# Performance work log

Measured on AMD Instinct MI355X. Metric: run time of the kernel, lower is better.

Reference implementation:

```python
import jax, jax.numpy as jnp
import numpy as np

WEIGHT_FACTOR = 0.8


def _pairwise_l2(f):
    # ||a-b|| via GEMM trick: ||a||^2 + ||b||^2 - 2 a.b, avoiding the [N,N,D] blowup.
    sqn = jnp.sum(f * f, axis=1)                      # [N]
    sq = sqn[:, None] + sqn[None, :] - 2.0 * (f @ f.T)  # [N,N]
    sq = jnp.maximum(sq, 0.0)
    pos = sq > 0
    # safe sqrt: subgradient 0 at zero distance (matches torch.norm at 0)
    return jnp.where(pos, jnp.sqrt(jnp.where(pos, sq, 1.0)), 0.0)


def _mse(a, b):
    d = a - b
    return jnp.mean(d * d)


def setup_inputs() -> dict:
    key = jax.random.key(0)
    ks = jax.random.split(key, 8)
    N, D, C = 4096, 256, 1000
    return {
        "pred": jax.random.normal(ks[0], (N, C), dtype=jnp.float32),
        "target": jax.random.normal(ks[1], (N, C), dtype=jnp.float32),
        "pred_f0": jax.random.normal(ks[2], (N, D), dtype=jnp.float32),
        "pred_f1": jax.random.normal(ks[3], (N, D), dtype=jnp.float32),
        "pred_f2": jax.random.normal(ks[4], (N, D), dtype=jnp.float32),
        "target_f0": jax.random.normal(ks[5], (N, D), dtype=jnp.float32),
        "target_f1": jax.random.normal(ks[6], (N, D), dtype=jnp.float32),
        "target_f2": jax.random.normal(ks[7], (N, D), dtype=jnp.float32),
    }


def reference(pred, target, pred_f0, pred_f1, pred_f2, target_f0, target_f1, target_f2):
    pred_feats = (pred_f0, pred_f1, pred_f2)
    target_feats = (target_f0, target_f1, target_f2)
    num_features = len(pred_feats)

    label_loss = _mse(pred, target)
    feature_loss = 0.0
    for pf, tf in zip(pred_feats, target_feats):
        feature_loss = feature_loss + _mse(_pairwise_l2(pf), _pairwise_l2(tf))
    return (1.0 - WEIGHT_FACTOR) * label_loss + WEIGHT_FACTOR * feature_loss / num_features
```

## Files before the change

kernel.cpp:

```cpp
#include <hip/hip_runtime.h>
#include <stdint.h>

#define NR 4096
#define DD 256
#define NC_TOT 4096000
#define TILES 32
#define NTRI 528
#define NBLK_GRAM 512

typedef float f32x4 __attribute__((ext_vector_type(4)));
typedef unsigned char u8;

#define WS_MSEP_OFF  256
#define WS_FEATP_OFF 16384
#define WS_SQN_OFF   32768
#define WS_FP8_OFF   131072

#define GBAR()     asm volatile("s_barrier" ::: "memory")
#define WAIT_VM(N) asm volatile("s_waitcnt vmcnt(" #N ")" ::: "memory")

__global__ __launch_bounds__(256) void prep_mse_kernel(
    const float* __restrict__ m0, const float* __restrict__ m1,
    const float* __restrict__ m2, const float* __restrict__ m3,
    const float* __restrict__ m4, const float* __restrict__ m5,
    const float4* __restrict__ pred, const float4* __restrict__ target,
    u8* __restrict__ q8, float* __restrict__ sqn, float* __restrict__ msep,
    unsigned* __restrict__ cnt)
{
    __shared__ float sr[4];
    const int t = threadIdx.x, w = t >> 6, lane = t & 63;
    const int y = blockIdx.y;
    if (y == 0 && blockIdx.x == 0 && t == 0) *cnt = 0u;

    if (y < 6) {
        const float* mp = m0;
        if (y == 1) mp = m1;
        else if (y == 2) mp = m2;
        else if (y == 3) mp = m3;
        else if (y == 4) mp = m4;
        else if (y == 5) mp = m5;
        const int R = blockIdx.x * 4 + w;
        const int P = R >> 7, rr = R & 127;
        const float4* src = (const float4*)(mp + (size_t)R * DD);
        float4 v = src[lane];
        float ss = v.x * v.x + v.y * v.y + v.z * v.z + v.w * v.w;
        unsigned lo = __builtin_amdgcn_cvt_pk_fp8_f32(v.x, v.y, 0u, false);
        unsigned hi = __builtin_amdgcn_cvt_pk_fp8_f32(v.z, v.w, 0u, false);
        unsigned packed = (lo & 0xffffu) | (hi << 16);
        size_t idx = ((size_t)(y * 32 + P) << 15)
                     + (size_t)(lane >> 1) * 1024 + rr * 8 + (lane & 1) * 4;
        *(unsigned*)(q8 + idx) = packed;
        #pragma unroll
        for (int off = 32; off; off >>= 1) ss += __shfl_down(ss, off);
        if (lane == 0) sqn[(size_t)y * NR + R] = ss;
    } else {
        const int b2 = (y - 6) * 1024 + blockIdx.x;
        float s = 0.f;
        for (int i = b2 * 256 + t; i < NC_TOT / 4; i += 2048 * 256) {
            float4 x = pred[i], yv = target[i];
            float dx = x.x - yv.x, dy = x.y - yv.y;
            float dz = x.z - yv.z, dw = x.w - yv.w;
            s += dx * dx + dy * dy + dz * dz + dw * dw;
        }
        #pragma unroll
        for (int off = 32; off; off >>= 1) s += __shfl_down(s, off);
        if (lane == 0) sr[w] = s;
        __syncthreads();
        if (t == 0) msep[b2] = sr[0] + sr[1] + sr[2] + sr[3];
    }
}

#define COMPUTE_STAGE(BI, ACC)                                                 \
  do {                                                                         \
    const u8* tA_ = &buf[BI][0];                                               \
    const u8* tB_ = &buf[BI][16384];                                           \
    __builtin_amdgcn_s_setprio(1);                                             \
    _Pragma("unroll")                                                          \
    for (int kc = 0; kc < 4; kc++) {                                           \
      const int gg = kc * 4 + quad;                                            \
      long a_[4], b_[2];                                                       \
      _Pragma("unroll")                                                        \
      for (int mi = 0; mi < 4; mi++)                                           \
        a_[mi] = *(const long*)&tA_[gg * 1024 + (wm * 64 + mi * 16 + l16) * 8];\
      _Pragma("unroll")                                                        \
      for (int ni = 0; ni < 2; ni++)                                           \
        b_[ni] = *(const long*)&tB_[gg * 1024 + (wn * 32 + ni * 16 + l16) * 8];\
      _Pragma("unroll")                                                        \
      for (int mi = 0; mi < 4; mi++)                                           \
        _Pragma("unroll")                                                      \
        for (int ni = 0; ni < 2; ni++)                                         \
          ACC[mi][ni] = __builtin_amdgcn_mfma_f32_16x16x32_fp8_fp8(            \
              a_[mi], b_[ni], ACC[mi][ni], 0, 0, 0);                           \
    }                                                                          \
    __builtin_amdgcn_s_setprio(0);                                             \
  } while (0)

#define RESET_ACC()                                                            \
  do {                                                                         \
    _Pragma("unroll")                                                          \
    for (int a4 = 0; a4 < 4; a4++)                                             \
      _Pragma("unroll")                                                        \
      for (int b2 = 0; b2 < 2; b2++) {                                         \
        accp[a4][b2] = f32x4{0.f, 0.f, 0.f, 0.f};                              \
        acct[a4][b2] = f32x4{0.f, 0.f, 0.f, 0.f};                              \
      }                                                                        \
  } while (0)

__global__ __launch_bounds__(512, 4) void gram_loss_kernel(
    const u8* __restrict__ q8, const float* __restrict__ sqn,
    float* __restrict__ featp, const float* __restrict__ msep,
    unsigned* __restrict__ cnt, float* __restrict__ out)
{
    __shared__ u8 buf[2][32768];
    __shared__ float s_red[8];
    __shared__ int s_last;

    const int xcd = blockIdx.x & 7, slot = blockIdx.x >> 3;
    const int t = threadIdx.x;
    const int w = t >> 6, lane = t & 63;
    const int wm = w >> 2, wn = w & 3;
    const int quad = lane >> 4, l16 = lane & 15;
    const char* qb = (const char*)q8;

    auto tile_of = [&](int k, int& f, int& ti, int& tj) -> bool {
        int rs = (slot + k * 21 + xcd * 9) & 63;
        int idx = rs + (k << 6), lin;
        if (xcd < 6) {
            if (idx >= 196) return false;
            f = xcd >> 1; lin = (xcd & 1) + 2 * idx;
        } else {
            if (idx >= 204) return false;
            int rr = (xcd - 6) + 2 * idx;
            f = rr / 136; lin = 392 + rr - f * 136;
        }
        int a = 0, rem = lin;
        while (rem >= TILES - a) { rem -= TILES - a; a++; }
        ti = a; tj = a + rem;
        return true;
    };

    auto prefetch = [&](int b, int f, int ti, int tj, int tgt, int kk) {
        const int m = f + 3 * tgt;
        const size_t bA = ((size_t)(m * 32 + ti)) << 15;
        const size_t bB = ((size_t)(m * 32 + tj)) << 15;
        const char* g = qb + ((w < 4) ? bA : bB) + kk * 16384
                        + (w & 3) * 4096 + lane * 16;
        char* l = (char*)&buf[b][0] + ((w < 4) ? 0 : 16384) + (w & 3) * 4096;
        #pragma unroll
        for (int i = 0; i < 4; i++)
            __builtin_amdgcn_global_load_lds(
                (const __attribute__((address_space(1))) void*)(g + i * 1024),
                (__attribute__((address_space(3))) void*)(l + i * 1024), 16, 0, 0);
    };

    f32x4 accp[4][2], acct[4][2];
    RESET_ACC();

    float local = 0.f;

    int fc, tic, tjc;
    tile_of(0, fc, tic, tjc);
    prefetch(0, fc, tic, tjc, 0, 0);
    prefetch(1, fc, tic, tjc, 0, 1);

    int k = 0;
    while (true) {
        WAIT_VM(4); GBAR();
        COMPUTE_STAGE(0, accp);
        GBAR();

        prefetch(0, fc, tic, tjc, 1, 0);
        WAIT_VM(4); GBAR();
        COMPUTE_STAGE(1, accp);
        GBAR();

        prefetch(1, fc, tic, tjc, 1, 1);
        WAIT_VM(4); GBAR();
        COMPUTE_STAGE(0, acct);
        GBAR();

        int fn, tin, tjn;
        const bool more = tile_of(k + 1, fn, tin, tjn);
        if (more) { prefetch(0, fn, tin, tjn, 0, 0); WAIT_VM(4); }
        else      { WAIT_VM(0); }
        GBAR();
        COMPUTE_STAGE(1, acct);
        GBAR();
        if (more) prefetch(1, fn, tin, tjn, 0, 1);

        {
            const float* sqp = sqn + (size_t)fc * NR;
            const float* sqt = sqn + (size_t)(3 + fc) * NR;
            const bool diag = (tic == tjc);
            float tl = 0.f;
            #pragma unroll
            for (int mi = 0; mi < 4; mi++) {
                const int i0 = wm * 64 + mi * 16 + quad * 4;
                const f32x4 sip = *(const f32x4*)(sqp + tic * 128 + i0);
                const f32x4 sit = *(const f32x4*)(sqt + tic * 128 + i0);
                #pragma unroll
                for (int ni = 0; ni < 2; ni++) {
                    const int j_loc = wn * 32 + ni * 16 + l16;
                    const float spj = sqp[tjc * 128 + j_loc];
                    const float stj = sqt[tjc * 128 + j_loc];
                    const f32x4 gp = accp[mi][ni], gt = acct[mi][ni];
                    #pragma unroll
                    for (int r = 0; r < 4; r++) {
                        float dp2 = fmaxf(fmaf(-2.f, gp[r], sip[r] + spj), 0.f);
                        float dt2 = fmaxf(fmaf(-2.f, gt[r], sit[r] + stj), 0.f);
                        if (diag && (i0 + r == j_loc)) { dp2 = 0.f; dt2 = 0.f; }
                        float sq = __builtin_amdgcn_sqrtf(dp2 * dt2);
                        tl += fmaf(-2.f, sq, dp2 + dt2);
                    }
                }
            }
            local += diag ? tl : 2.f * tl;
            RESET_ACC();
        }
        if (!more) break;
        k++;
        fc = fn; tic = tin; tjc = tjn;
    }

    #pragma unroll
    for (int off = 32; off; off >>= 1) local += __shfl_down(local, off);
    if (lane == 0) s_red[w] = local;
    __syncthreads();
    if (t == 0) {
        float bs = 0.f;
        #pragma unroll
        for (int i = 0; i < 8; i++) bs += s_red[i];
        featp[blockIdx.x] = bs;
        __threadfence();
        unsigned old = atomicAdd(cnt, 1u);
        s_last = (old == NBLK_GRAM - 1) ? 1 : 0;
    }
    __syncthreads();

    if (s_last) {
        __threadfence();
        float s2 = 0.f, m2 = 0.f;
        for (int i = t; i < NBLK_GRAM; i += 512) s2 += featp[i];
        for (int i = t; i < 2048; i += 512) m2 += msep[i];
        #pragma unroll
        for (int off = 32; off; off >>= 1) {
            s2 += __shfl_down(s2, off);
            m2 += __shfl_down(m2, off);
        }
        __shared__ float fr[8], mr[8];
        if (lane == 0) { fr[w] = s2; mr[w] = m2; }
        __syncthreads();
        if (t == 0) {
            float fs = 0.f, ms = 0.f;
            #pragma unroll
            for (int i = 0; i < 8; i++) { fs += fr[i]; ms += mr[i]; }
            out[0] = 0.2f * (ms / (float)NC_TOT) +
                     (0.8f / 3.0f) * (fs / ((float)NR * (float)NR));
        }
    }
}

extern "C" void kernel_launch(void* const* d_in, const int* in_sizes, int n_in,
                              void* d_out, int out_size, void* d_ws, size_t ws_size,
                              hipStream_t stream) {
    unsigned* cnt  = (unsigned*)d_ws;
    float* msep    = (float*)((char*)d_ws + WS_MSEP_OFF);
    float* featp   = (float*)((char*)d_ws + WS_FEATP_OFF);
    float* sqn     = (float*)((char*)d_ws + WS_SQN_OFF);
    u8* q8         = (u8*)((char*)d_ws + WS_FP8_OFF);

    prep_mse_kernel<<<dim3(1024, 8), 256, 0, stream>>>(
        (const float*)d_in[2], (const float*)d_in[3], (const float*)d_in[4],
        (const float*)d_in[5], (const float*)d_in[6], (const float*)d_in[7],
        (const float4*)d_in[0], (const float4*)d_in[1], q8, sqn, msep, cnt);

    gram_loss_kernel<<<NBLK_GRAM, 512, 0, stream>>>(
        q8, sqn, featp, msep, cnt, (float*)d_out);
}
```

Baseline: 142.4 us.

## Split gram tiles into 128x64 halves with 256-thread blocks and 768 blocks

```diff
diff --git a/kernel.cpp b/kernel.cpp
--- a/kernel.cpp
+++ b/kernel.cpp
@@ -6,7 +6,7 @@
 #define NC_TOT 4096000
 #define TILES 32
 #define NTRI 528
-#define NBLK_GRAM 512
+#define NBLK_GRAM 768
 
 typedef float f32x4 __attribute__((ext_vector_type(4)));
 typedef unsigned char u8;
@@ -84,7 +84,7 @@
         a_[mi] = *(const long*)&tA_[gg * 1024 + (wm * 64 + mi * 16 + l16) * 8];\
       _Pragma("unroll")                                                        \
       for (int ni = 0; ni < 2; ni++)                                           \
-        b_[ni] = *(const long*)&tB_[gg * 1024 + (wn * 32 + ni * 16 + l16) * 8];\
+        b_[ni] = *(const long*)&tB_[gg * 512 + (wn * 32 + ni * 16 + l16) * 8]; \
       _Pragma("unroll")                                                        \
       for (int mi = 0; mi < 4; mi++)                                           \
         _Pragma("unroll")                                                      \
@@ -106,51 +106,59 @@
       }                                                                        \
   } while (0)
 
-__global__ __launch_bounds__(512, 4) void gram_loss_kernel(
+__global__ __launch_bounds__(256, 4) void gram_loss_kernel(
     const u8* __restrict__ q8, const float* __restrict__ sqn,
     float* __restrict__ featp, const float* __restrict__ msep,
     unsigned* __restrict__ cnt, float* __restrict__ out)
 {
-    __shared__ u8 buf[2][32768];
-    __shared__ float s_red[8];
+    __shared__ u8 buf[2][24576];
+    __shared__ float s_red[4];
     __shared__ int s_last;
 
     const int xcd = blockIdx.x & 7, slot = blockIdx.x >> 3;
     const int t = threadIdx.x;
     const int w = t >> 6, lane = t & 63;
-    const int wm = w >> 2, wn = w & 3;
+    const int wm = w >> 1, wn = w & 1;
     const int quad = lane >> 4, l16 = lane & 15;
     const char* qb = (const char*)q8;
 
-    auto tile_of = [&](int k, int& f, int& ti, int& tj) -> bool {
-        int rs = (slot + k * 21 + xcd * 9) & 63;
-        int idx = rs + (k << 6), lin;
+    auto tile_of = [&](int k, int& f, int& ti, int& tj, int& h) -> bool {
+        int rs = (slot + k * 37 + xcd * 11) % 96;
+        int idx = rs + k * 96, lin;
         if (xcd < 6) {
-            if (idx >= 196) return false;
-            f = xcd >> 1; lin = (xcd & 1) + 2 * idx;
+            if (idx >= 392) return false;
+            f = xcd >> 1; lin = (xcd & 1) + 2 * (idx >> 1);
         } else {
-            if (idx >= 204) return false;
-            int rr = (xcd - 6) + 2 * idx;
+            if (idx >= 408) return false;
+            int rr = (xcd - 6) + 2 * (idx >> 1);
             f = rr / 136; lin = 392 + rr - f * 136;
         }
+        h = idx & 1;
         int a = 0, rem = lin;
         while (rem >= TILES - a) { rem -= TILES - a; a++; }
         ti = a; tj = a + rem;
         return true;
     };
 
-    auto prefetch = [&](int b, int f, int ti, int tj, int tgt, int kk) {
+    auto prefetch = [&](int b, int f, int ti, int tj, int tgt, int kk, int h) {
         const int m = f + 3 * tgt;
         const size_t bA = ((size_t)(m * 32 + ti)) << 15;
         const size_t bB = ((size_t)(m * 32 + tj)) << 15;
-        const char* g = qb + ((w < 4) ? bA : bB) + kk * 16384
-                        + (w & 3) * 4096 + lane * 16;
-        char* l = (char*)&buf[b][0] + ((w < 4) ? 0 : 16384) + (w & 3) * 4096;
+        const char* gA = qb + bA + kk * 16384 + w * 4096 + lane * 16;
+        char* lA = (char*)&buf[b][0] + w * 4096;
         #pragma unroll
         for (int i = 0; i < 4; i++)
             __builtin_amdgcn_global_load_lds(
-                (const __attribute__((address_space(1))) void*)(g + i * 1024),
-                (__attribute__((address_space(3))) void*)(l + i * 1024), 16, 0, 0);
+                (const __attribute__((address_space(1))) void*)(gA + i * 1024),
+                (__attribute__((address_space(3))) void*)(lA + i * 1024), 16, 0, 0);
+        const char* gB = qb + bB + ((size_t)(kk * 16 + 4 * w) << 10)
+                         + (lane >> 5) * 1024 + h * 512 + (lane & 31) * 16;
+        char* lB = (char*)&buf[b][16384] + w * 2048;
+        #pragma unroll
+        for (int i = 0; i < 2; i++)
+            __builtin_amdgcn_global_load_lds(
+                (const __attribute__((address_space(1))) void*)(gB + i * 2048),
+                (__attribute__((address_space(3))) void*)(lB + i * 1024), 16, 0, 0);
     };
 
     f32x4 accp[4][2], acct[4][2];
@@ -158,35 +166,35 @@
 
     float local = 0.f;
 
-    int fc, tic, tjc;
-    tile_of(0, fc, tic, tjc);
-    prefetch(0, fc, tic, tjc, 0, 0);
-    prefetch(1, fc, tic, tjc, 0, 1);
+    int fc, tic, tjc, hc;
+    tile_of(0, fc, tic, tjc, hc);
+    prefetch(0, fc, tic, tjc, 0, 0, hc);
+    prefetch(1, fc, tic, tjc, 0, 1, hc);
 
     int k = 0;
     while (true) {
-        WAIT_VM(4); GBAR();
+        WAIT_VM(6); GBAR();
         COMPUTE_STAGE(0, accp);
         GBAR();
 
-        prefetch(0, fc, tic, tjc, 1, 0);
-        WAIT_VM(4); GBAR();
+        prefetch(0, fc, tic, tjc, 1, 0, hc);
+        WAIT_VM(6); GBAR();
         COMPUTE_STAGE(1, accp);
         GBAR();
 
-        prefetch(1, fc, tic, tjc, 1, 1);
-        WAIT_VM(4); GBAR();
+        prefetch(1, fc, tic, tjc, 1, 1, hc);
+        WAIT_VM(6); GBAR();
         COMPUTE_STAGE(0, acct);
         GBAR();
 
-        int fn, tin, tjn;
-        const bool more = tile_of(k + 1, fn, tin, tjn);
-        if (more) { prefetch(0, fn, tin, tjn, 0, 0); WAIT_VM(4); }
+        int fn, tin, tjn, hn;
+        const bool more = tile_of(k + 1, fn, tin, tjn, hn);
+        if (more) { prefetch(0, fn, tin, tjn, 0, 0, hn); WAIT_VM(6); }
         else      { WAIT_VM(0); }
         GBAR();
         COMPUTE_STAGE(1, acct);
         GBAR();
-        if (more) prefetch(1, fn, tin, tjn, 0, 1);
+        if (more) prefetch(1, fn, tin, tjn, 0, 1, hn);
 
         {
             const float* sqp = sqn + (size_t)fc * NR;
@@ -201,14 +209,15 @@
                 #pragma unroll
                 for (int ni = 0; ni < 2; ni++) {
                     const int j_loc = wn * 32 + ni * 16 + l16;
-                    const float spj = sqp[tjc * 128 + j_loc];
-                    const float stj = sqt[tjc * 128 + j_loc];
+                    const int j_col = hc * 64 + j_loc;
+                    const float spj = sqp[tjc * 128 + j_col];
+                    const float stj = sqt[tjc * 128 + j_col];
                     const f32x4 gp = accp[mi][ni], gt = acct[mi][ni];
                     #pragma unroll
                     for (int r = 0; r < 4; r++) {
                         float dp2 = fmaxf(fmaf(-2.f, gp[r], sip[r] + spj), 0.f);
                         float dt2 = fmaxf(fmaf(-2.f, gt[r], sit[r] + stj), 0.f);
-                        if (diag && (i0 + r == j_loc)) { dp2 = 0.f; dt2 = 0.f; }
+                        if (diag && (i0 + r == j_col)) { dp2 = 0.f; dt2 = 0.f; }
                         float sq = __builtin_amdgcn_sqrtf(dp2 * dt2);
                         tl += fmaf(-2.f, sq, dp2 + dt2);
                     }
@@ -219,7 +228,7 @@
         }
         if (!more) break;
         k++;
-        fc = fn; tic = tin; tjc = tjn;
+        fc = fn; tic = tin; tjc = tjn; hc = hn;
     }
 
     #pragma unroll
@@ -229,7 +238,7 @@
     if (t == 0) {
         float bs = 0.f;
         #pragma unroll
-        for (int i = 0; i < 8; i++) bs += s_red[i];
+        for (int i = 0; i < 4; i++) bs += s_red[i];
         featp[blockIdx.x] = bs;
         __threadfence();
         unsigned old = atomicAdd(cnt, 1u);
@@ -240,20 +249,20 @@
     if (s_last) {
         __threadfence();
         float s2 = 0.f, m2 = 0.f;
-        for (int i = t; i < NBLK_GRAM; i += 512) s2 += featp[i];
-        for (int i = t; i < 2048; i += 512) m2 += msep[i];
+        for (int i = t; i < NBLK_GRAM; i += 256) s2 += featp[i];
+        for (int i = t; i < 2048; i += 256) m2 += msep[i];
         #pragma unroll
         for (int off = 32; off; off >>= 1) {
             s2 += __shfl_down(s2, off);
             m2 += __shfl_down(m2, off);
         }
-        __shared__ float fr[8], mr[8];
+        __shared__ float fr[4], mr[4];
         if (lane == 0) { fr[w] = s2; mr[w] = m2; }
         __syncthreads();
         if (t == 0) {
             float fs = 0.f, ms = 0.f;
             #pragma unroll
-            for (int i = 0; i < 8; i++) { fs += fr[i]; ms += mr[i]; }
+            for (int i = 0; i < 4; i++) { fs += fr[i]; ms += mr[i]; }
             out[0] = 0.2f * (ms / (float)NC_TOT) +
                      (0.8f / 3.0f) * (fs / ((float)NR * (float)NR));
         }
@@ -274,6 +283,6 @@
         (const float*)d_in[5], (const float*)d_in[6], (const float*)d_in[7],
         (const float4*)d_in[0], (const float4*)d_in[1], q8, sqn, msep, cnt);
 
-    gram_loss_kernel<<<NBLK_GRAM, 512, 0, stream>>>(
+    gram_loss_kernel<<<NBLK_GRAM, 256, 0, stream>>>(
         q8, sqn, featp, msep, cnt, (float*)d_out);
 }
```

After: 164.4 us. +15.5%, slower.
